# Kernel tuning notes

Hardware: AMD Instinct MI355X
Metric: run time of the kernel (lower is better)

## Reference

```python
import jax, jax.numpy as jnp
import numpy as np

HEADS = 8

def setup_inputs() -> dict:
    key = jax.random.key(0)
    ks = jax.random.split(key, 10)
    B, S, E = 2, 2048, 512
    q = jax.random.normal(ks[0], (B, S, E), jnp.float32)
    k = jax.random.normal(ks[1], (B, S, E), jnp.float32)
    v = jax.random.normal(ks[2], (B, S, E), jnp.float32)
    mask = jnp.zeros((S, S), jnp.float32)  # additive mask [s_q, s_k]
    scale = 0.02
    Wq = jax.random.normal(ks[3], (E, E), jnp.float32) * scale
    bq = jax.random.normal(ks[4], (E,), jnp.float32) * scale
    Wk = jax.random.normal(ks[5], (E, E), jnp.float32) * scale
    bk = jax.random.normal(ks[6], (E,), jnp.float32) * scale
    Wv = jax.random.normal(ks[7], (E, E), jnp.float32) * scale
    bv = jax.random.normal(ks[8], (E,), jnp.float32) * scale
    return {"q": q, "k": k, "v": v, "mask": mask,
            "Wq": Wq, "bq": bq, "Wk": Wk, "bk": bk, "Wv": Wv, "bv": bv}

def reference(q, k, v, mask, Wq, bq, Wk, bk, Wv, bv):
    H = HEADS
    b, s_q, _ = q.shape
    s_k = k.shape[1]
    s_v = v.shape[1]
    # NOTE: faithful to source: row-major view(b, H, s, -1) WITHOUT transposing
    # seq/head axes first (quirk of the original module).
    K = jnp.swapaxes((k @ Wk.T + bk).reshape(b, H, s_k, -1), 2, 3)  # [b,H,dh,s_k]
    Q = (q @ Wq.T + bq).reshape(b, H, s_q, -1)                      # [b,H,s_q,dh]
    V = (v @ Wv.T + bv).reshape(b, H, s_v, -1)                      # [b,H,s_v,dh]
    # NOTE: original scales by sqrt(K.shape[-1]) AFTER the transpose, i.e. sqrt(s_k)
    scores = (Q @ K) / jnp.sqrt(jnp.asarray(s_k, jnp.float32))      # [b,H,s_q,s_k]
    scores = scores + mask[:s_q, :s_k]
    attn = jax.nn.softmax(scores, axis=-1)
    out = (attn @ V).reshape(b, s_q, -1)  # [b, s_q, e]
    return out
```

## Files before the change

### kernel.cpp

```cpp
#include <hip/hip_runtime.h>


#define SEQ 2048
#define EMB 512
#define DH  64
#define MROWS 4096
#define NROWS 32768

typedef float  v4f __attribute__((ext_vector_type(4)));
typedef short  v8s __attribute__((ext_vector_type(8)));
typedef __fp16 v2h __attribute__((ext_vector_type(2)));

static __device__ __forceinline__ unsigned int f2bf(float f) {
    unsigned int u = __float_as_uint(f);
    u += 0x7fffu + ((u >> 16) & 1u);
    return u >> 16;
}
static __device__ __forceinline__ unsigned int pack2(float a, float b) {
    return f2bf(a) | (f2bf(b) << 16);
}
static __device__ __forceinline__ unsigned int packh2(float a, float b) {
    v2h h = __builtin_amdgcn_cvt_pkrtz(a, b);
    return __builtin_bit_cast(unsigned int, h);
}

__global__ __launch_bounds__(256, 3) void proj_kernel(
    const float* __restrict__ q, const float* __restrict__ k, const float* __restrict__ v,
    const float* __restrict__ Wq, const float* __restrict__ bq,
    const float* __restrict__ Wk, const float* __restrict__ bk,
    const float* __restrict__ Wv, const float* __restrict__ bv,
    const float* __restrict__ mask,
    unsigned short* __restrict__ Qbf, unsigned short* __restrict__ Kbf,
    unsigned short* __restrict__ Vbf, float* __restrict__ maskT,
    unsigned int* __restrict__ flags)
{
    __shared__ __align__(16) char smem[27648];
    const int tid = threadIdx.x;

    if (blockIdx.x >= 768) {
        const int mb2 = blockIdx.x - 768;
        const int rb = mb2 >> 5, kt = mb2 & 31;
        float* tile = maskT + ((size_t)rb * 32 + kt) * 8192;
        float4 vals[8];
        bool any = false;
#pragma unroll
        for (int i = 0; i < 8; ++i) {
            int s = tid + i * 256;
            int l  = s & 63;
            int cb = (s >> 6) & 3;
            int g  = (s >> 8) & 1;
            int w2 = (s >> 9) & 3;
            int qd2 = l >> 4, n2 = l & 15;
            vals[i] = *(const float4*)&mask[
                (size_t)(rb * 128 + w2 * 32 + g * 16 + n2) * SEQ + kt * 64 + cb * 16 + qd2 * 4];
            any = any | (vals[i].x != 0.f) | (vals[i].y != 0.f)
                      | (vals[i].z != 0.f) | (vals[i].w != 0.f);
        }
        unsigned int* nzp = (unsigned int*)smem;
        if (tid == 0) *nzp = 0u;
        __syncthreads();
        if (any) *nzp = 1u;
        __syncthreads();
        if (*nzp) {
#pragma unroll
            for (int i = 0; i < 8; ++i) {
                int s = tid + i * 256;
                *(float4*)&tile[(size_t)s * 4] = vals[i];
            }
            if (tid == 0) atomicOr(&flags[rb], 1u << kt);
        }
        return;
    }

    char* As = smem;
    char* Ws = smem + 9216;

    const int id  = blockIdx.x;
    const int pos = id & 31;
    const int nb  = pos >> 3;
    const int unit = (id >> 5) * 8 + (pos & 7);
    const int mb = unit & 63;
    const int z  = unit >> 6;

    const float* A    = (z == 0) ? q  : (z == 1) ? k  : v;
    const float* W    = (z == 0) ? Wq : (z == 1) ? Wk : Wv;
    const float* bias = (z == 0) ? bq : (z == 1) ? bk : bv;
    unsigned short* Cg = (z == 0) ? Qbf : (z == 1) ? Kbf : Vbf;

    const int w    = tid >> 6;
    const int lane = tid & 63;
    const int qd   = lane >> 4;
    const int n    = lane & 15;
    const int m0 = mb * 64, n0 = nb * 128;

    float4 areg[4], wreg[8];
#pragma unroll
    for (int i = 0; i < 4; ++i) {
        int c = tid + i * 256;
        areg[i] = *(const float4*)&A[(size_t)(m0 + (c >> 4)) * EMB + (c & 15) * 4];
    }
#pragma unroll
    for (int i = 0; i < 8; ++i) {
        int c = tid + i * 256;
        wreg[i] = *(const float4*)&W[(size_t)(n0 + (c >> 4)) * EMB + (c & 15) * 4];
    }

    v4f acc[8];
#pragma unroll
    for (int cb = 0; cb < 8; ++cb) acc[cb] = (v4f)0.f;

#pragma unroll 1
    for (int kt = 0; kt < 8; ++kt) {
        __syncthreads();
#pragma unroll
        for (int i = 0; i < 4; ++i) {
            int c = tid + i * 256;
            uint2 pk = { pack2(areg[i].x, areg[i].y), pack2(areg[i].z, areg[i].w) };
            *(uint2*)&As[(c >> 4) * 144 + (c & 15) * 8] = pk;
        }
#pragma unroll
        for (int i = 0; i < 8; ++i) {
            int c = tid + i * 256;
            uint2 pk = { pack2(wreg[i].x, wreg[i].y), pack2(wreg[i].z, wreg[i].w) };
            *(uint2*)&Ws[(c >> 4) * 144 + (c & 15) * 8] = pk;
        }
        __syncthreads();

        if (kt + 1 < 8) {
#pragma unroll
            for (int i = 0; i < 4; ++i) {
                int c = tid + i * 256;
                areg[i] = *(const float4*)&A[(size_t)(m0 + (c >> 4)) * EMB + (kt+1) * 64 + (c & 15) * 4];
            }
#pragma unroll
            for (int i = 0; i < 8; ++i) {
                int c = tid + i * 256;
                wreg[i] = *(const float4*)&W[(size_t)(n0 + (c >> 4)) * EMB + (kt+1) * 64 + (c & 15) * 4];
            }
        }

#pragma unroll
        for (int ks = 0; ks < 2; ++ks) {
            v8s af = *(const v8s*)&As[(w * 16 + n) * 144 + ks * 64 + qd * 16];
#pragma unroll
            for (int cb = 0; cb < 8; ++cb) {
                v8s bfr = *(const v8s*)&Ws[(cb * 16 + n) * 144 + ks * 64 + qd * 16];
                acc[cb] = __builtin_amdgcn_mfma_f32_16x16x32_bf16(af, bfr, acc[cb], 0, 0, 0);
            }
        }
    }

    const float osc = (z == 0) ? 0.02209708691207961f : 1.0f;
    float bb[8];
#pragma unroll
    for (int cb = 0; cb < 8; ++cb) bb[cb] = bias[n0 + cb * 16 + n];
#pragma unroll
    for (int cb = 0; cb < 8; ++cb)
#pragma unroll
        for (int r = 0; r < 4; ++r) acc[cb][r] = (acc[cb][r] + bb[cb]) * osc;

    __syncthreads();
    short* Ct = (short*)smem;
#pragma unroll
    for (int cb = 0; cb < 8; ++cb)
#pragma unroll
        for (int r = 0; r < 4; ++r)
            Ct[(w * 16 + qd * 4 + r) * 136 + cb * 16 + n] = (short)f2bf(acc[cb][r]);
    __syncthreads();
    const int rr = tid >> 2, q4 = tid & 3;
#pragma unroll
    for (int i = 0; i < 4; ++i) {
        uint4 t4 = *(const uint4*)&smem[rr * 272 + q4 * 64 + i * 16];
        *(uint4*)&Cg[(size_t)(m0 + rr) * EMB + n0 + q4 * 32 + i * 8] = t4;
    }
}

__global__ __launch_bounds__(256) void vtrans_kernel(
    const unsigned short* __restrict__ Vbf, unsigned short* __restrict__ VtT)
{
    __shared__ unsigned short T[64 * 136];
    const int bh = blockIdx.x, kt = blockIdx.y;
    const int tid = threadIdx.x;
    const unsigned short* Vh = Vbf + (size_t)bh * (SEQ * DH) + (size_t)kt * 64 * DH;
#pragma unroll
    for (int i = 0; i < 2; ++i) {
        int c = tid + i * 256;
        int s_l = c >> 3, ch = c & 7;
        uint4 t4 = *(const uint4*)&Vh[c * 8];
        const unsigned short* e = (const unsigned short*)&t4;
#pragma unroll
        for (int j = 0; j < 8; ++j)
            T[(ch * 8 + j) * 136 + s_l] = e[j];
    }
    __syncthreads();
    unsigned short* Ot = VtT + ((size_t)bh * 32 + kt) * (64 * 64);
    const int d = tid >> 2, sq = tid & 3;
#pragma unroll
    for (int i = 0; i < 2; ++i) {
        uint4 t4 = *(const uint4*)&T[d * 136 + sq * 16 + i * 8];
        *(uint4*)&Ot[d * 64 + sq * 16 + i * 8] = t4;
    }
}

template <int SPLITS>
__global__ __launch_bounds__(256, 4) void attn_kernel(
    const unsigned short* __restrict__ Qbf, const unsigned short* __restrict__ Kbf,
    const unsigned short* __restrict__ VtT,
    const float* __restrict__ maskT, const float* __restrict__ maskf,
    const unsigned int* __restrict__ flags,
    unsigned short* __restrict__ Opart, float* __restrict__ ml,
    float* __restrict__ out)
{
    __shared__ __align__(16) char smem[36864];
    char* Ks  = smem;
    char* Vts = smem + 9216;

    const int tid  = threadIdx.x;
    const int w    = tid >> 6;
    const int lane = tid & 63;
    const int qd   = lane >> 4;
    const int n    = lane & 15;
    char* Ps = smem + 18432 + w * 4608;

    const int id = blockIdx.x;
    const int bh = (id & 7) * 2 + ((id >> 3) & 1);
    const int unit = id >> 4;
    const int rb = unit & 15;
    const int kq = unit >> 4;
    const int KT0 = kq * (32 / SPLITS), KT1 = KT0 + 32 / SPLITS;

    const unsigned short* Qh = Qbf + (size_t)bh * (SEQ * DH);
    const unsigned short* Kh = Kbf + (size_t)bh * (SEQ * DH);
    const unsigned short* Vth = VtT + (size_t)bh * 32 * 4096;

    const unsigned int fl = (SPLITS > 1) ? flags[rb] : 0u;

    v8s qf[2][2];
#pragma unroll
    for (int g = 0; g < 2; ++g) {
        const size_t qrow = (size_t)(rb * 128 + w * 32 + g * 16 + n);
#pragma unroll
        for (int ks = 0; ks < 2; ++ks)
            qf[g][ks] = *(const v8s*)&Qh[qrow * DH + ks * 32 + qd * 8];
    }

    uint4 kreg[2], vreg[2];
#pragma unroll
    for (int p = 0; p < 2; ++p) {
        int c = tid + p * 256;
        kreg[p] = *(const uint4*)&Kh[(size_t)KT0 * 4096 + c * 8];
        vreg[p] = *(const uint4*)&Vth[(size_t)KT0 * 4096 + c * 8];
    }

    float l_[2] = { 0.f, 0.f };
    v4f oacc[2][4];
#pragma unroll
    for (int g = 0; g < 2; ++g)
#pragma unroll
        for (int cb = 0; cb < 4; ++cb) oacc[g][cb] = (v4f)0.f;

#pragma unroll 1
    for (int kt = KT0; kt < KT1; ++kt) {
        __syncthreads();
#pragma unroll
        for (int p = 0; p < 2; ++p) {
            int c = tid + p * 256;
            *(uint4*)&Ks [(c >> 3) * 144 + (c & 7) * 16] = kreg[p];
            *(uint4*)&Vts[(c >> 3) * 144 + (c & 7) * 16] = vreg[p];
        }
        __syncthreads();

        v4f sacc[2][4];
        float4 mk[2][4];
        if (SPLITS > 1) {
            if (fl & (1u << kt)) {
                const float* tileF = maskT + ((size_t)rb * 32 + kt) * 8192;
#pragma unroll
                for (int g = 0; g < 2; ++g)
#pragma unroll
                    for (int cb = 0; cb < 4; ++cb)
                        sacc[g][cb] = *(const v4f*)&tileF[
                            (size_t)((((w * 2 + g) * 4 + cb) * 64) + qd * 16 + n) * 4];
            } else {
#pragma unroll
                for (int g = 0; g < 2; ++g)
#pragma unroll
                    for (int cb = 0; cb < 4; ++cb) sacc[g][cb] = (v4f)0.f;
            }
        } else {
#pragma unroll
            for (int g = 0; g < 2; ++g) {
                const size_t mrow = (size_t)(rb * 128 + w * 32 + g * 16 + n);
#pragma unroll
                for (int cb = 0; cb < 4; ++cb) {
                    mk[g][cb] = *(const float4*)&maskf[mrow * SEQ + kt * 64 + cb * 16 + qd * 4];
                    sacc[g][cb] = (v4f)0.f;
                }
            }
        }

        if (kt + 1 < KT1) {
#pragma unroll
            for (int p = 0; p < 2; ++p) {
                int c = tid + p * 256;
                kreg[p] = *(const uint4*)&Kh[(size_t)(kt + 1) * 4096 + c * 8];
                vreg[p] = *(const uint4*)&Vth[(size_t)(kt + 1) * 4096 + c * 8];
            }
        }

#pragma unroll
        for (int ks = 0; ks < 2; ++ks)
#pragma unroll
            for (int cb = 0; cb < 4; ++cb) {
                v8s kf = *(const v8s*)&Ks[(cb * 16 + n) * 144 + ks * 64 + qd * 16];
#pragma unroll
                for (int g = 0; g < 2; ++g)
                    sacc[g][cb] = __builtin_amdgcn_mfma_f32_16x16x32_bf16(kf, qf[g][ks], sacc[g][cb], 0, 0, 0);
            }

#pragma unroll
        for (int g = 0; g < 2; ++g) {
            float rs = 0.f;
            float pv[4][4];
#pragma unroll
            for (int cb = 0; cb < 4; ++cb) {
                if (SPLITS == 1) {
                    sacc[g][cb][0] += mk[g][cb].x; sacc[g][cb][1] += mk[g][cb].y;
                    sacc[g][cb][2] += mk[g][cb].z; sacc[g][cb][3] += mk[g][cb].w;
                }
#pragma unroll
                for (int r = 0; r < 4; ++r) {
                    float e = __expf(sacc[g][cb][r]);
                    pv[cb][r] = e;
                    rs += e;
                }
            }
            rs += __shfl_xor(rs, 16);
            rs += __shfl_xor(rs, 32);
            l_[g] += rs;
#pragma unroll
            for (int cb = 0; cb < 4; ++cb) {
                uint2 pk = { pack2(pv[cb][0], pv[cb][1]), pack2(pv[cb][2], pv[cb][3]) };
                *(uint2*)&Ps[(g * 16 + n) * 144 + cb * 32 + qd * 8] = pk;
            }
        }

#pragma unroll
        for (int ks = 0; ks < 2; ++ks) {
            v8s pf[2];
#pragma unroll
            for (int g = 0; g < 2; ++g)
                pf[g] = *(const v8s*)&Ps[(g * 16 + n) * 144 + ks * 64 + qd * 16];
#pragma unroll
            for (int cb = 0; cb < 4; ++cb) {
                v8s vf = *(const v8s*)&Vts[(cb * 16 + n) * 144 + ks * 64 + qd * 16];
#pragma unroll
                for (int g = 0; g < 2; ++g)
                    oacc[g][cb] = __builtin_amdgcn_mfma_f32_16x16x32_bf16(vf, pf[g], oacc[g][cb], 0, 0, 0);
            }
        }
    }

    if (SPLITS == 1) {
#pragma unroll
        for (int g = 0; g < 2; ++g) {
            const float inv = 1.0f / l_[g];
#pragma unroll
            for (int cb = 0; cb < 4; ++cb)
#pragma unroll
                for (int r = 0; r < 4; ++r) oacc[g][cb][r] *= inv;
        }
    } else {
        if (qd == 0) {
#pragma unroll
            for (int g = 0; g < 2; ++g) {
                const size_t row = (size_t)bh * SEQ + rb * 128 + w * 32 + g * 16 + n;
                ml[(size_t)kq * NROWS + row] = l_[g];
            }
        }
    }
    __syncthreads();
#pragma unroll
    for (int g = 0; g < 2; ++g)
#pragma unroll
        for (int cb = 0; cb < 4; ++cb)
            *(v4f*)&smem[(w * 32 + g * 16 + n) * 272 + cb * 64 + qd * 16] = oacc[g][cb];
    __syncthreads();
    const int r_l = tid >> 1, hf = tid & 1;
    if (SPLITS == 1) {
        float* dst = &out[((size_t)bh * SEQ + rb * 128 + r_l) * DH + hf * 32];
#pragma unroll
        for (int i = 0; i < 8; ++i) {
            float4 t4 = *(const float4*)&smem[r_l * 272 + hf * 128 + i * 16];
            *(float4*)&dst[i * 4] = t4;
        }
    } else {
        unsigned short* dst = &Opart[((size_t)kq * NROWS + (size_t)bh * SEQ + rb * 128 + r_l) * DH + hf * 32];
#pragma unroll
        for (int i = 0; i < 4; ++i) {
            float4 f0 = *(const float4*)&smem[r_l * 272 + hf * 128 + i * 32];
            float4 f1 = *(const float4*)&smem[r_l * 272 + hf * 128 + i * 32 + 16];
            uint4 o = { packh2(f0.x, f0.y), packh2(f0.z, f0.w),
                        packh2(f1.x, f1.y), packh2(f1.z, f1.w) };
            *(uint4*)&dst[i * 8] = o;
        }
    }
}

__global__ __launch_bounds__(256) void combine_kernel(
    const unsigned int* __restrict__ Opart, const float* __restrict__ ml,
    float* __restrict__ out, int splits)
{
    const int tid = threadIdx.x;
    const size_t row = (size_t)blockIdx.x * 16 + (tid >> 4);
    const int d4 = (tid & 15) * 4;
    float denom = 0.f;
    float4 o = make_float4(0.f, 0.f, 0.f, 0.f);
    for (int s = 0; s < splits; ++s) {
        denom += ml[(size_t)s * NROWS + row];
        uint2 u = *(const uint2*)&Opart[((size_t)s * NROWS + row) * 32 + (d4 >> 1)];
        v2h h0 = __builtin_bit_cast(v2h, u.x);
        v2h h1 = __builtin_bit_cast(v2h, u.y);
        o.x += (float)h0.x; o.y += (float)h0.y;
        o.z += (float)h1.x; o.w += (float)h1.y;
    }
    const float inv = 1.0f / denom;
    o.x *= inv; o.y *= inv; o.z *= inv; o.w *= inv;
    *(float4*)&out[row * DH + d4] = o;
}

extern "C" void kernel_launch(void* const* d_in, const int* in_sizes, int n_in,
                              void* d_out, int out_size, void* d_ws, size_t ws_size,
                              hipStream_t stream) {
    const float* q    = (const float*)d_in[0];
    const float* k    = (const float*)d_in[1];
    const float* v    = (const float*)d_in[2];
    const float* mask = (const float*)d_in[3];
    const float* Wq   = (const float*)d_in[4];
    const float* bq   = (const float*)d_in[5];
    const float* Wk   = (const float*)d_in[6];
    const float* bk   = (const float*)d_in[7];
    const float* Wv   = (const float*)d_in[8];
    const float* bv   = (const float*)d_in[9];

    char* ws = (char*)d_ws;
    const size_t MB = 1024 * 1024;
    unsigned short* Qbf   = (unsigned short*)(ws + 0);
    unsigned short* Kbf   = (unsigned short*)(ws + 4 * MB);
    unsigned short* VtT   = (unsigned short*)(ws + 8 * MB);
    unsigned short* Opart = (unsigned short*)(ws + 12 * MB);
    unsigned short* Vbf   = (unsigned short*)(ws + 12 * MB);
    float*          mlp   = (float*)(ws + 28 * MB);
    unsigned int*   flags = (unsigned int*)(ws + 28 * MB + 512 * 1024);
    float*          maskT = (float*)(ws + 29 * MB);

    const size_t need_split = 45 * MB;
    const bool do_split = ws_size >= need_split;

    if (do_split) {
        (void)hipMemsetAsync(flags, 0, 64, stream);
        proj_kernel<<<1280, 256, 0, stream>>>(q, k, v, Wq, bq, Wk, bk, Wv, bv,
                                              mask, Qbf, Kbf, Vbf, maskT, flags);
        dim3 tgrid(16, 32);
        vtrans_kernel<<<tgrid, 256, 0, stream>>>(Vbf, VtT);
        attn_kernel<4><<<1024, 256, 0, stream>>>(Qbf, Kbf, VtT, maskT, mask, flags,
                                                 Opart, mlp, (float*)d_out);
        combine_kernel<<<NROWS / 16, 256, 0, stream>>>((const unsigned int*)Opart,
                                                       mlp, (float*)d_out, 4);
    } else {
        proj_kernel<<<768, 256, 0, stream>>>(q, k, v, Wq, bq, Wk, bk, Wv, bv,
                                             mask, Qbf, Kbf, Vbf, maskT, flags);
        dim3 tgrid(16, 32);
        vtrans_kernel<<<tgrid, 256, 0, stream>>>(Vbf, VtT);
        attn_kernel<1><<<256, 256, 0, stream>>>(Qbf, Kbf, VtT, maskT, mask, flags,
                                                Opart, mlp, (float*)d_out);
    }
}
```

Measured before the change: 174.6 us.

## Halve attention query tile to 64 rows and alias P buffer onto K tile

Result: slower. 219.9 us (+25.9%).

```diff
diff --git a/kernel.cpp b/kernel.cpp
--- a/kernel.cpp
+++ b/kernel.cpp
@@ -203,7 +203,7 @@
 }
 
 template <int SPLITS>
-__global__ __launch_bounds__(256, 4) void attn_kernel(
+__global__ __launch_bounds__(256, 8) void attn_kernel(
     const unsigned short* __restrict__ Qbf, const unsigned short* __restrict__ Kbf,
     const unsigned short* __restrict__ VtT,
     const float* __restrict__ maskT, const float* __restrict__ maskf,
@@ -211,7 +211,7 @@
     unsigned short* __restrict__ Opart, float* __restrict__ ml,
     float* __restrict__ out)
 {
-    __shared__ __align__(16) char smem[36864];
+    __shared__ __align__(16) char smem[18432];
     char* Ks  = smem;
     char* Vts = smem + 9216;
 
@@ -220,28 +220,27 @@
     const int lane = tid & 63;
     const int qd   = lane >> 4;
     const int n    = lane & 15;
-    char* Ps = smem + 18432 + w * 4608;
+    char* Ps = smem + w * 2304;
 
     const int id = blockIdx.x;
     const int bh = (id & 7) * 2 + ((id >> 3) & 1);
     const int unit = id >> 4;
-    const int rb = unit & 15;
-    const int kq = unit >> 4;
+    const int rb6 = unit & 31;
+    const int kq = unit >> 5;
     const int KT0 = kq * (32 / SPLITS), KT1 = KT0 + 32 / SPLITS;
 
     const unsigned short* Qh = Qbf + (size_t)bh * (SEQ * DH);
     const unsigned short* Kh = Kbf + (size_t)bh * (SEQ * DH);
     const unsigned short* Vth = VtT + (size_t)bh * 32 * 4096;
 
-    const unsigned int fl = (SPLITS > 1) ? flags[rb] : 0u;
-
-    v8s qf[2][2];
-#pragma unroll
-    for (int g = 0; g < 2; ++g) {
-        const size_t qrow = (size_t)(rb * 128 + w * 32 + g * 16 + n);
+    const unsigned int fl = (SPLITS > 1) ? flags[rb6 >> 1] : 0u;
+
+    v8s qf[2];
+    {
+        const size_t qrow = (size_t)(rb6 * 64 + w * 16 + n);
 #pragma unroll
         for (int ks = 0; ks < 2; ++ks)
-            qf[g][ks] = *(const v8s*)&Qh[qrow * DH + ks * 32 + qd * 8];
+            qf[ks] = *(const v8s*)&Qh[qrow * DH + ks * 32 + qd * 8];
     }
 
     uint4 kreg[2], vreg[2];
@@ -252,12 +251,10 @@
         vreg[p] = *(const uint4*)&Vth[(size_t)KT0 * 4096 + c * 8];
     }
 
-    float l_[2] = { 0.f, 0.f };
-    v4f oacc[2][4];
-#pragma unroll
-    for (int g = 0; g < 2; ++g)
-#pragma unroll
-        for (int cb = 0; cb < 4; ++cb) oacc[g][cb] = (v4f)0.f;
+    float l_ = 0.f;
+    v4f oacc[4];
+#pragma unroll
+    for (int cb = 0; cb < 4; ++cb) oacc[cb] = (v4f)0.f;
 
 #pragma unroll 1
     for (int kt = KT0; kt < KT1; ++kt) {
@@ -270,32 +267,26 @@
         }
         __syncthreads();
 
-        v4f sacc[2][4];
-        float4 mk[2][4];
+        v4f sacc[4];
+        float4 mk[4];
         if (SPLITS > 1) {
             if (fl & (1u << kt)) {
-                const float* tileF = maskT + ((size_t)rb * 32 + kt) * 8192;
-#pragma unroll
-                for (int g = 0; g < 2; ++g)
-#pragma unroll
-                    for (int cb = 0; cb < 4; ++cb)
-                        sacc[g][cb] = *(const v4f*)&tileF[
-                            (size_t)((((w * 2 + g) * 4 + cb) * 64) + qd * 16 + n) * 4];
+                const float* tileF = maskT + ((size_t)(rb6 >> 1) * 32 + kt) * 8192;
+                const int wg = (rb6 & 1) * 4 + w;
+#pragma unroll
+                for (int cb = 0; cb < 4; ++cb)
+                    sacc[cb] = *(const v4f*)&tileF[
+                        (size_t)((wg * 4 + cb) * 64 + qd * 16 + n) * 4];
             } else {
 #pragma unroll
-                for (int g = 0; g < 2; ++g)
-#pragma unroll
-                    for (int cb = 0; cb < 4; ++cb) sacc[g][cb] = (v4f)0.f;
+                for (int cb = 0; cb < 4; ++cb) sacc[cb] = (v4f)0.f;
             }
         } else {
-#pragma unroll
-            for (int g = 0; g < 2; ++g) {
-                const size_t mrow = (size_t)(rb * 128 + w * 32 + g * 16 + n);
-#pragma unroll
-                for (int cb = 0; cb < 4; ++cb) {
-                    mk[g][cb] = *(const float4*)&maskf[mrow * SEQ + kt * 64 + cb * 16 + qd * 4];
-                    sacc[g][cb] = (v4f)0.f;
-                }
+            const size_t mrow = (size_t)(rb6 * 64 + w * 16 + n);
+#pragma unroll
+            for (int cb = 0; cb < 4; ++cb) {
+                mk[cb] = *(const float4*)&maskf[mrow * SEQ + kt * 64 + cb * 16 + qd * 4];
+                sacc[cb] = (v4f)0.f;
             }
         }
 
@@ -313,93 +304,78 @@
 #pragma unroll
             for (int cb = 0; cb < 4; ++cb) {
                 v8s kf = *(const v8s*)&Ks[(cb * 16 + n) * 144 + ks * 64 + qd * 16];
-#pragma unroll
-                for (int g = 0; g < 2; ++g)
-                    sacc[g][cb] = __builtin_amdgcn_mfma_f32_16x16x32_bf16(kf, qf[g][ks], sacc[g][cb], 0, 0, 0);
-            }
-
-#pragma unroll
-        for (int g = 0; g < 2; ++g) {
+                sacc[cb] = __builtin_amdgcn_mfma_f32_16x16x32_bf16(kf, qf[ks], sacc[cb], 0, 0, 0);
+            }
+        __syncthreads();
+
+        {
             float rs = 0.f;
             float pv[4][4];
 #pragma unroll
             for (int cb = 0; cb < 4; ++cb) {
                 if (SPLITS == 1) {
-                    sacc[g][cb][0] += mk[g][cb].x; sacc[g][cb][1] += mk[g][cb].y;
-                    sacc[g][cb][2] += mk[g][cb].z; sacc[g][cb][3] += mk[g][cb].w;
+                    sacc[cb][0] += mk[cb].x; sacc[cb][1] += mk[cb].y;
+                    sacc[cb][2] += mk[cb].z; sacc[cb][3] += mk[cb].w;
                 }
 #pragma unroll
                 for (int r = 0; r < 4; ++r) {
-                    float e = __expf(sacc[g][cb][r]);
+                    float e = __expf(sacc[cb][r]);
                     pv[cb][r] = e;
                     rs += e;
                 }
             }
             rs += __shfl_xor(rs, 16);
             rs += __shfl_xor(rs, 32);
-            l_[g] += rs;
+            l_ += rs;
 #pragma unroll
             for (int cb = 0; cb < 4; ++cb) {
                 uint2 pk = { pack2(pv[cb][0], pv[cb][1]), pack2(pv[cb][2], pv[cb][3]) };
-                *(uint2*)&Ps[(g * 16 + n) * 144 + cb * 32 + qd * 8] = pk;
+                *(uint2*)&Ps[n * 144 + cb * 32 + qd * 8] = pk;
             }
         }
 
 #pragma unroll
         for (int ks = 0; ks < 2; ++ks) {
-            v8s pf[2];
-#pragma unroll
-            for (int g = 0; g < 2; ++g)
-                pf[g] = *(const v8s*)&Ps[(g * 16 + n) * 144 + ks * 64 + qd * 16];
+            v8s pf = *(const v8s*)&Ps[n * 144 + ks * 64 + qd * 16];
 #pragma unroll
             for (int cb = 0; cb < 4; ++cb) {
                 v8s vf = *(const v8s*)&Vts[(cb * 16 + n) * 144 + ks * 64 + qd * 16];
-#pragma unroll
-                for (int g = 0; g < 2; ++g)
-                    oacc[g][cb] = __builtin_amdgcn_mfma_f32_16x16x32_bf16(vf, pf[g], oacc[g][cb], 0, 0, 0);
+                oacc[cb] = __builtin_amdgcn_mfma_f32_16x16x32_bf16(vf, pf, oacc[cb], 0, 0, 0);
             }
         }
     }
 
     if (SPLITS == 1) {
-#pragma unroll
-        for (int g = 0; g < 2; ++g) {
-            const float inv = 1.0f / l_[g];
-#pragma unroll
-            for (int cb = 0; cb < 4; ++cb)
-#pragma unroll
-                for (int r = 0; r < 4; ++r) oacc[g][cb][r] *= inv;
-        }
+        const float inv = 1.0f / l_;
+#pragma unroll
+        for (int cb = 0; cb < 4; ++cb)
+#pragma unroll
+            for (int r = 0; r < 4; ++r) oacc[cb][r] *= inv;
     } else {
         if (qd == 0) {
-#pragma unroll
-            for (int g = 0; g < 2; ++g) {
-                const size_t row = (size_t)bh * SEQ + rb * 128 + w * 32 + g * 16 + n;
-                ml[(size_t)kq * NROWS + row] = l_[g];
-            }
+            const size_t row = (size_t)bh * SEQ + rb6 * 64 + w * 16 + n;
+            ml[(size_t)kq * NROWS + row] = l_;
         }
     }
     __syncthreads();
 #pragma unroll
-    for (int g = 0; g < 2; ++g)
-#pragma unroll
-        for (int cb = 0; cb < 4; ++cb)
-            *(v4f*)&smem[(w * 32 + g * 16 + n) * 272 + cb * 64 + qd * 16] = oacc[g][cb];
+    for (int cb = 0; cb < 4; ++cb)
+        *(v4f*)&smem[(w * 16 + n) * 272 + cb * 64 + qd * 16] = oacc[cb];
     __syncthreads();
-    const int r_l = tid >> 1, hf = tid & 1;
+    const int r_l = tid >> 2, q4 = tid & 3;
     if (SPLITS == 1) {
-        float* dst = &out[((size_t)bh * SEQ + rb * 128 + r_l) * DH + hf * 32];
-#pragma unroll
-        for (int i = 0; i < 8; ++i) {
-            float4 t4 = *(const float4*)&smem[r_l * 272 + hf * 128 + i * 16];
+        float* dst = &out[((size_t)bh * SEQ + rb6 * 64 + r_l) * DH + q4 * 16];
+#pragma unroll
+        for (int i = 0; i < 4; ++i) {
+            float4 t4 = *(const float4*)&smem[r_l * 272 + q4 * 64 + i * 16];
             *(float4*)&dst[i * 4] = t4;
         }
     } else {
-        unsigned short* dst = &Opart[((size_t)kq * NROWS + (size_t)bh * SEQ + rb * 128 + r_l) * DH + hf * 32];
-#pragma unroll
-        for (int i = 0; i < 4; ++i) {
-            float4 f0 = *(const float4*)&smem[r_l * 272 + hf * 128 + i * 32];
-            float4 f1 = *(const float4*)&smem[r_l * 272 + hf * 128 + i * 32 + 16];
+        unsigned short* dst = &Opart[((size_t)kq * NROWS + (size_t)bh * SEQ + rb6 * 64 + r_l) * DH + q4 * 16];
+#pragma unroll
+        for (int i = 0; i < 2; ++i) {
+            float4 f0 = *(const float4*)&smem[r_l * 272 + q4 * 64 + i * 32];
+            float4 f1 = *(const float4*)&smem[r_l * 272 + q4 * 64 + i * 32 + 16];
             uint4 o = { packh2(f0.x, f0.y), packh2(f0.z, f0.w),
                         packh2(f1.x, f1.y), packh2(f1.z, f1.w) };
             *(uint4*)&dst[i * 8] = o;
@@ -463,7 +439,7 @@
                                               mask, Qbf, Kbf, Vbf, maskT, flags);
         dim3 tgrid(16, 32);
         vtrans_kernel<<<tgrid, 256, 0, stream>>>(Vbf, VtT);
-        attn_kernel<4><<<1024, 256, 0, stream>>>(Qbf, Kbf, VtT, maskT, mask, flags,
+        attn_kernel<4><<<2048, 256, 0, stream>>>(Qbf, Kbf, VtT, maskT, mask, flags,
                                                  Opart, mlp, (float*)d_out);
         combine_kernel<<<NROWS / 16, 256, 0, stream>>>((const unsigned int*)Opart,
                                                        mlp, (float*)d_out, 4);
@@ -472,7 +448,7 @@
                                              mask, Qbf, Kbf, Vbf, maskT, flags);
         dim3 tgrid(16, 32);
         vtrans_kernel<<<tgrid, 256, 0, stream>>>(Vbf, VtT);
-        attn_kernel<1><<<256, 256, 0, stream>>>(Qbf, Kbf, VtT, maskT, mask, flags,
+        attn_kernel<1><<<512, 256, 0, stream>>>(Qbf, Kbf, VtT, maskT, mask, flags,
                                                 Opart, mlp, (float*)d_out);
     }
 }
```
